# Kernel optimization log

Hardware: AMD Instinct MI355X
Metric: run time of the kernel (lower is better)

## Reference

```python
import jax, jax.numpy as jnp
import numpy as np

T, B, N, D, H = 12, 32, 64, 2, 128
HID, HEAD = 32, 4          # GATBlock n_hid, n_head; HEAD*HID == H
M = N * (N - 1)            # edge rows per get_graph
N_ACT = N - 1              # active nodes per batch row


def _make_graph():
    rec = np.zeros((M, N), np.float32)
    snd = np.zeros((M, N), np.float32)
    k = np.arange(N_ACT * N_ACT)
    ii = np.repeat(np.arange(N_ACT), N_ACT)
    jj = np.tile(np.arange(N_ACT), N_ACT)
    snd[k, ii] = 1.0
    rec[k, jj] = 1.0
    return rec, snd


def setup_inputs() -> dict:
    key = jax.random.key(0)
    ks = jax.random.split(key, 16)
    rec, snd = _make_graph()
    inp = {
        "inputs": jax.random.normal(ks[0], (T, B, N, D), jnp.float32),
        "hidden": jax.random.normal(ks[1], (B, N, H), jnp.float32),
        "rel_rec": jnp.asarray(np.broadcast_to(rec, (B, M, N)).copy()),
        "rel_send": jnp.asarray(np.broadcast_to(snd, (B, M, N)).copy()),
        # GATBlock rn1: fc1(D->HID), fc2(2*HID->HEAD)
        "rn1_W1": jax.random.normal(ks[2], (HID, D)) * 0.1,
        "rn1_b1": jnp.zeros((HID,)),
        "rn1_W2": jax.random.normal(ks[3], (HEAD, 2 * HID)) * 0.1,
        "rn1_b2": jnp.zeros((HEAD,)),
        # GATBlock rn2: fc1(H->HID), fc2(2*HID->HEAD)
        "rn2_W1": jax.random.normal(ks[4], (HID, H)) * 0.1,
        "rn2_b1": jnp.zeros((HID,)),
        "rn2_W2": jax.random.normal(ks[5], (HEAD, 2 * HID)) * 0.1,
        "rn2_b2": jnp.zeros((HEAD,)),
        # GRUCell(H, H)
        "gru_Wih": jax.random.normal(ks[6], (3 * H, H)) * 0.05,
        "gru_Whh": jax.random.normal(ks[7], (3 * H, H)) * 0.05,
        "gru_bih": jnp.zeros((3 * H,)),
        "gru_bhh": jnp.zeros((3 * H,)),
        # out Linear(H, D)
        "out_W": jax.random.normal(ks[8], (D, H)) * 0.1,
        "out_b": jnp.zeros((D,)),
    }
    return inp


def _gat_block(x_in, rel_rec, rel_send, W1, b1, W2, b2):
    # x_in: B x N x Din
    x = x_in @ W1.T + b1                                   # B,N,HID
    s = jnp.einsum('bmn,bnd->bmd', rel_send, x)            # B,M,HID (senders)
    r = jnp.einsum('bmn,bnd->bmd', rel_rec, x)             # B,M,HID (receivers)
    a = jax.nn.elu(jnp.concatenate([s, r], -1) @ W2.T + b2)  # B,M,HEAD
    # per-receiving-node masked softmax over the edge dim (edge2node)
    m = rel_rec[..., None] > 0                             # B,M,N,1
    logits = jnp.where(m, a[:, :, None, :], -jnp.inf)      # B,M,N,HEAD
    mx = jnp.max(logits, axis=1, keepdims=True)
    mx = jnp.where(jnp.isfinite(mx), mx, 0.0)
    e = jnp.where(m, jnp.exp(logits - mx), 0.0)
    denom = jnp.sum(e, axis=1, keepdims=True)
    att = e / jnp.where(denom > 0, denom, 1.0)             # B,M,N,HEAD
    # weighted scatter-sum: outer(att_edge, sender_feat) summed per node
    out = jnp.einsum('bmnh,bmd->bnhd', att, s)             # B,N,HEAD,HID
    Bn, Nn = x_in.shape[0], x_in.shape[1]
    return jax.nn.elu(out.reshape(Bn, Nn, HEAD * HID))     # B,N,H


def _gru_cell(x, h, Wih, Whh, bih, bhh):
    gi = x @ Wih.T + bih
    gh = h @ Whh.T + bhh
    i_r, i_z, i_n = jnp.split(gi, 3, axis=-1)
    h_r, h_z, h_n = jnp.split(gh, 3, axis=-1)
    r = jax.nn.sigmoid(i_r + h_r)
    z = jax.nn.sigmoid(i_z + h_z)
    n = jnp.tanh(i_n + r * h_n)
    return (1.0 - z) * n + z * h


def reference(inputs, hidden, rel_rec, rel_send,
              rn1_W1, rn1_b1, rn1_W2, rn1_b2,
              rn2_W1, rn2_b1, rn2_W2, rn2_b2,
              gru_Wih, gru_Whh, gru_bih, gru_bhh,
              out_W, out_b):
    def step(h, x_t):
        x = _gat_block(x_t, rel_rec, rel_send, rn1_W1, rn1_b1, rn1_W2, rn1_b2)
        h = _gru_cell(x, h, gru_Wih, gru_Whh, gru_bih, gru_bhh)
        h = _gat_block(h, rel_rec, rel_send, rn2_W1, rn2_b1, rn2_W2, rn2_b2)
        return h, None
    h_final, _ = jax.lax.scan(step, hidden, inputs)
    pred = h_final @ out_W.T + out_b                       # B,N,D
    return pred
```

## Files before the change

### kernel.cpp

```cpp
#include <hip/hip_runtime.h>


#define T_   12
#define B_   32
#define N_   64
#define D_   2
#define H_   128
#define HID_ 32
#define HEAD_ 4
#define NA_  63

__device__ __forceinline__ float eluf(float x){ return x>0.f ? x : expm1f(x); }

#define OFF_H    0u
#define OFF_X1   262144u
#define OFF_PS1  1048576u
#define OFF_PR1  1146880u
#define OFF_XG   1245184u
#define OFF_X2   4390912u
#define OFF_PS2  4456448u
#define OFF_PR2  4464640u
#define OFF_WT   OFF_X1
#define OFF_GI   4472832u
#define WS_NEED_A ((4472832ull + 9437184ull) * 4ull)

__global__ void gat1_fc(const float* __restrict__ inp, const float* __restrict__ W1,
                        const float* __restrict__ b1, const float* __restrict__ W2,
                        const float* __restrict__ b2,
                        float* __restrict__ x1_all, float* __restrict__ ps_all,
                        float* __restrict__ pr_all){
  int grp = blockIdx.x;
  int tid = threadIdx.x;
  __shared__ float sx1[N_*HID_];
  __shared__ float sW1[HID_*D_];
  __shared__ float sb1[HID_];
  __shared__ float sW2[HEAD_*2*HID_];
  __shared__ float sxin[N_*D_];
  if(tid < 64)  sW1[tid] = W1[tid];
  if(tid < 32)  sb1[tid] = b1[tid];
  sW2[tid] = W2[tid];
  if(tid < 128) sxin[tid] = inp[grp*N_*D_ + tid];
  __syncthreads();
  for(int o = tid; o < N_*HID_; o += 256){
    int n = o >> 5, k = o & 31;
    float v = sb1[k] + sxin[n*2]*sW1[k*2] + sxin[n*2+1]*sW1[k*2+1];
    sx1[o] = v;
    x1_all[grp*N_*HID_ + o] = v;
  }
  __syncthreads();
  for(int p = tid; p < N_*8; p += 256){
    int n = p >> 3, q = p & 7, hh = q & 3;
    const float* w  = sW2 + hh*64 + ((q < 4) ? 0 : 32);
    const float* xr = sx1 + n*32;
    float acc = (q < 4) ? b2[hh] : 0.f;
    #pragma unroll
    for(int c = 0; c < 32; c++) acc += xr[c]*w[c];
    if(q < 4) ps_all[grp*N_*HEAD_ + n*4 + hh] = acc;
    else      pr_all[grp*N_*HEAD_ + n*4 + hh] = acc;
  }
}

__global__ void prep_wt(const float* __restrict__ Wih, const float* __restrict__ Whh,
                        float* __restrict__ wtb){
  int idx = blockIdx.x*256 + threadIdx.x;
  int k4 = idx / 768, j = idx - k4*768;
  const float* src = (j < 384) ? (Wih + (size_t)j*H_) : (Whh + (size_t)(j-384)*H_);
  ((float4*)wtb)[idx] = ((const float4*)src)[k4];
}

__global__ __launch_bounds__(256) void gat_att_big2(const float* __restrict__ x1,
    const float* __restrict__ ps, const float* __restrict__ pr,
    float* __restrict__ out){
  int blk = blockIdx.x, g = blk >> 1, dh = blk & 1, tid = threadIdx.x;
  __shared__ float sX[N_*HID_];
  __shared__ float sPs[N_*HEAD_];
  __shared__ float sPr[N_*HEAD_];
  {
    const float4* xs = (const float4*)(x1 + (size_t)g*(N_*HID_));
    ((float4*)sX)[tid]       = xs[tid];
    ((float4*)sX)[tid + 256] = xs[tid + 256];
    sPs[tid] = ps[g*(N_*HEAD_) + tid];
    sPr[tid] = pr[g*(N_*HEAD_) + tid];
  }
  __syncthreads();
  float* outg = out + (size_t)g*(N_*H_);
  if(tid < NA_*HEAD_){
    int r = tid, hh = r & 3;
    float prv = sPr[r];
    float tmax = -1e30f;
    for(int i = 0; i < NA_; i++) tmax = fmaxf(tmax, sPs[i*4 + hh]);
    float m = eluf(tmax + prv);
    float4 acc[4];
    #pragma unroll
    for(int k = 0; k < 4; k++) acc[k] = make_float4(0.f,0.f,0.f,0.f);
    float s = 0.f;
    #pragma unroll 3
    for(int i = 0; i < NA_; i++){
      float tt = sPs[i*4 + hh] + prv;
      float v = tt > 0.f ? tt : expm1f(tt);
      float p = expf(v - m);
      s += p;
      const float4* sxp = (const float4*)&sX[i*32 + dh*16];
      #pragma unroll
      for(int k = 0; k < 4; k++){
        float4 xv = sxp[k];
        acc[k].x += p*xv.x; acc[k].y += p*xv.y;
        acc[k].z += p*xv.z; acc[k].w += p*xv.w;
      }
    }
    float inv = 1.f/s;
    float4* orow = (float4*)(outg + (r>>2)*H_ + hh*32 + dh*16);
    #pragma unroll
    for(int k = 0; k < 4; k++){
      float4 o;
      o.x = eluf(acc[k].x*inv); o.y = eluf(acc[k].y*inv);
      o.z = eluf(acc[k].z*inv); o.w = eluf(acc[k].w*inv);
      orow[k] = o;
    }
  } else {
    int hh = tid - NA_*HEAD_;
    float4 z4 = make_float4(0.f,0.f,0.f,0.f);
    float4* zp = (float4*)(outg + NA_*H_ + hh*32 + dh*16);
    zp[0]=z4; zp[1]=z4; zp[2]=z4; zp[3]=z4;
  }
}

__global__ __launch_bounds__(256) void gi_gemm4(const float* __restrict__ xg,
    const float* __restrict__ wtb, float* __restrict__ gi){
  int tid = threadIdx.x;
  int r0 = blockIdx.x * 16;
  __shared__ __align__(16) float sxg[16][H_];
  ((float4*)sxg)[tid]       = ((const float4*)(xg + (size_t)r0*H_))[tid];
  ((float4*)sxg)[tid + 256] = ((const float4*)(xg + (size_t)r0*H_))[tid + 256];
  __syncthreads();
  int c = tid & 127, rh = (tid >> 7) * 8;
  const float4* wt4 = (const float4*)wtb;
  float ar[8]={0,0,0,0,0,0,0,0}, az[8]={0,0,0,0,0,0,0,0}, an[8]={0,0,0,0,0,0,0,0};
  #pragma unroll 2
  for(int k4 = 0; k4 < 32; k4++){
    float4 w0 = wt4[k4*768 + c];
    float4 w1 = wt4[k4*768 + 128 + c];
    float4 w2 = wt4[k4*768 + 256 + c];
    #pragma unroll
    for(int rr = 0; rr < 8; rr++){
      float4 xv = ((const float4*)sxg[rh + rr])[k4];
      ar[rr] += w0.x*xv.x + w0.y*xv.y + w0.z*xv.z + w0.w*xv.w;
      az[rr] += w1.x*xv.x + w1.y*xv.y + w1.z*xv.z + w1.w*xv.w;
      an[rr] += w2.x*xv.x + w2.y*xv.y + w2.z*xv.z + w2.w*xv.w;
    }
  }
  #pragma unroll
  for(int rr = 0; rr < 8; rr++){
    size_t base = (size_t)(r0 + rh + rr)*384;
    gi[base + c]       = ar[rr];
    gi[base + 128 + c] = az[rr];
    gi[base + 256 + c] = an[rr];
  }
}

__global__ __launch_bounds__(512) void gru_fc6(
    const float* __restrict__ gi, const float* __restrict__ hidden0, int t0,
    const float* __restrict__ x2prev, const float* __restrict__ psprev,
    const float* __restrict__ prprev,
    const float* __restrict__ wtb,
    const float* __restrict__ bih, const float* __restrict__ bhh,
    const float* __restrict__ W1, const float* __restrict__ b1,
    const float* __restrict__ W2, const float* __restrict__ b2,
    float* __restrict__ x2, float* __restrict__ ps2, float* __restrict__ pr2){
  int tid = threadIdx.x, blk = blockIdx.x;
  int g0 = blk*8, g = blk>>3, jbase = (blk&7)*8;
  __shared__ __align__(16) float sX[N_*HID_];
  __shared__ float sPs[N_*HEAD_];
  __shared__ __align__(16) float sh[8][H_];
  __shared__ __align__(16) float shn[8][H_];
  __shared__ float spart[4][24][H_];
  __shared__ float sx2[8][HID_];

  int c = tid & 127, rg = tid >> 7;
  const float4* wt4 = (const float4*)wtb;
  float4 wreg[8][3];
  #pragma unroll
  for(int kk = 0; kk < 8; kk++){
    const float4* wk = wt4 + (size_t)(rg*8 + kk)*768 + 384 + c;
    wreg[kk][0] = wk[0]; wreg[kk][1] = wk[128]; wreg[kk][2] = wk[256];
  }

  if(t0){
    if(tid < 256) ((float4*)sh)[tid] = ((const float4*)(hidden0 + (size_t)g0*H_))[tid];
  } else {
    ((float4*)sX)[tid] = ((const float4*)(x2prev + (size_t)g*(N_*HID_)))[tid];
    if(tid < 256) sPs[tid] = psprev[g*(N_*HEAD_) + tid];
  }
  __syncthreads();

  if(!t0){
    int rl = tid >> 4, l16 = tid & 15;
    int hh = rl & 3, jrow = rl >> 2;
    int jl = jbase + jrow;
    float prv = prprev[g*(N_*HEAD_) + jbase*4 + rl];
    float tmax = -1e30f;
    for(int i = 0; i < NA_; i++) tmax = fmaxf(tmax, sPs[i*4 + hh]);
    float m = eluf(tmax + prv);
    float a0 = 0.f, a1 = 0.f, s = 0.f;
    #pragma unroll 3
    for(int i = 0; i < NA_; i++){
      float tt = sPs[i*4 + hh] + prv;
      float v = tt > 0.f ? tt : expm1f(tt);
      float p = expf(v - m);
      s += p;
      const float2 xv = *(const float2*)&sX[i*32 + l16*2];
      a0 += p*xv.x; a1 += p*xv.y;
    }
    float inv = 1.f/s;
    float h0 = (jl == NA_) ? 0.f : eluf(a0*inv);
    float h1 = (jl == NA_) ? 0.f : eluf(a1*inv);
    sh[jrow][hh*32 + l16*2]     = h0;
    sh[jrow][hh*32 + l16*2 + 1] = h1;
  }
  __syncthreads();

  {
    float ar[8] = {0,0,0,0,0,0,0,0};
    float az[8] = {0,0,0,0,0,0,0,0};
    float an[8] = {0,0,0,0,0,0,0,0};
    #pragma unroll
    for(int kk = 0; kk < 8; kk++){
      int k4 = rg*8 + kk;
      #pragma unroll
      for(int r = 0; r < 8; r++){
        float4 hv = ((const float4*)sh[r])[k4];
        ar[r] += wreg[kk][0].x*hv.x + wreg[kk][0].y*hv.y + wreg[kk][0].z*hv.z + wreg[kk][0].w*hv.w;
        az[r] += wreg[kk][1].x*hv.x + wreg[kk][1].y*hv.y + wreg[kk][1].z*hv.z + wreg[kk][1].w*hv.w;
        an[r] += wreg[kk][2].x*hv.x + wreg[kk][2].y*hv.y + wreg[kk][2].z*hv.z + wreg[kk][2].w*hv.w;
      }
    }
    #pragma unroll
    for(int r = 0; r < 8; r++){
      spart[rg][r][c]      = ar[r];
      spart[rg][8 + r][c]  = az[r];
      spart[rg][16 + r][c] = an[r];
    }
  }
  __syncthreads();

  {
    float bi_r = bih[c], bi_z = bih[c+H_], bi_n = bih[c+2*H_];
    float bh_r = bhh[c], bh_z = bhh[c+H_], bh_n = bhh[c+2*H_];
    int r0 = rg*2;
    #pragma unroll
    for(int rr = 0; rr < 2; rr++){
      int r = r0 + rr;
      float hr = spart[0][r][c] + spart[1][r][c] + spart[2][r][c] + spart[3][r][c] + bh_r;
      float hz = spart[0][8+r][c] + spart[1][8+r][c] + spart[2][8+r][c] + spart[3][8+r][c] + bh_z;
      float hn = spart[0][16+r][c] + spart[1][16+r][c] + spart[2][16+r][c] + spart[3][16+r][c] + bh_n;
      const float* gir = gi + (size_t)(g0+r)*384;
      float ir  = gir[c]     + bi_r;
      float iz  = gir[c+128] + bi_z;
      float in_ = gir[c+256] + bi_n;
      float rgt = 1.f/(1.f+expf(-(ir+hr)));
      float zgt = 1.f/(1.f+expf(-(iz+hz)));
      float ngt = tanhf(in_ + rgt*hn);
      shn[r][c] = (1.f-zgt)*ngt + zgt*sh[r][c];
    }
  }
  __syncthreads();

  if(tid < 256){
    int r = tid >> 5, jc = tid & 31;
    const float4* wrow = (const float4*)(W1 + (size_t)jc*H_);
    const float4* hnr = (const float4*)shn[r];
    float acc = b1[jc];
    #pragma unroll 8
    for(int k4 = 0; k4 < 32; k4++){
      float4 w = wrow[k4], hv = hnr[k4];
      acc += w.x*hv.x + w.y*hv.y + w.z*hv.z + w.w*hv.w;
    }
    sx2[r][jc] = acc;
    x2[(size_t)(g0+r)*HID_ + jc] = acc;
  }
  __syncthreads();
  if(tid < 64){
    int r = tid >> 3, q = tid & 7, hh = q & 3;
    int base = (q < 4) ? 0 : 32;
    float acc = (q < 4) ? b2[hh] : 0.f;
    #pragma unroll
    for(int cc = 0; cc < 32; cc++) acc += sx2[r][cc]*W2[hh*64 + base + cc];
    if(q < 4) ps2[(g0+r)*HEAD_ + hh] = acc;
    else      pr2[(g0+r)*HEAD_ + hh] = acc;
  }
}

__global__ __launch_bounds__(512) void gru_fc3(
    const float* __restrict__ xg, const float* __restrict__ h,
    const float* __restrict__ wtb,
    const float* __restrict__ bih, const float* __restrict__ bhh,
    const float* __restrict__ W1, const float* __restrict__ b1,
    const float* __restrict__ W2, const float* __restrict__ b2,
    float* __restrict__ x2, float* __restrict__ ps2, float* __restrict__ pr2){
  int tid = threadIdx.x;
  int g0 = blockIdx.x * 8;
  __shared__ __align__(16) float sx[8][H_];
  __shared__ __align__(16) float sh[8][H_];
  __shared__ __align__(16) float shn[8][H_];
  __shared__ float sx2[8][HID_];
  if(tid < 256) ((float4*)sx)[tid]     = ((const float4*)(xg + (size_t)g0*H_))[tid];
  else          ((float4*)sh)[tid-256] = ((const float4*)(h  + (size_t)g0*H_))[tid-256];
  __syncthreads();
  int c = tid & 127, rg = tid >> 7, r0 = rg*2;
  const float4* wt4 = (const float4*)wtb;
  const float4* xr0 = (const float4*)sx[r0];
  const float4* xr1 = (const float4*)sx[r0+1];
  const float4* hp0 = (const float4*)sh[r0];
  const float4* hp1 = (const float4*)sh[r0+1];
  float air[2]={0,0}, aiz[2]={0,0}, ain[2]={0,0};
  float ahr[2]={0,0}, ahz[2]={0,0}, ahn[2]={0,0};
  #pragma unroll 2
  for(int k4 = 0; k4 < 32; k4++){
    const float4* wk = wt4 + k4*768 + c;
    float4 w0 = wk[0],   w1 = wk[128], w2 = wk[256];
    float4 w3 = wk[384], w4 = wk[512], w5 = wk[640];
    float4 xv0 = xr0[k4], xv1 = xr1[k4];
    float4 hv0 = hp0[k4], hv1 = hp1[k4];
    air[0] += w0.x*xv0.x + w0.y*xv0.y + w0.z*xv0.z + w0.w*xv0.w;
    aiz[0] += w1.x*xv0.x + w1.y*xv0.y + w1.z*xv0.z + w1.w*xv0.w;
    ain[0] += w2.x*xv0.x + w2.y*xv0.y + w2.z*xv0.z + w2.w*xv0.w;
    ahr[0] += w3.x*hv0.x + w3.y*hv0.y + w3.z*hv0.z + w3.w*hv0.w;
    ahz[0] += w4.x*hv0.x + w4.y*hv0.y + w4.z*hv0.z + w4.w*hv0.w;
    ahn[0] += w5.x*hv0.x + w5.y*hv0.y + w5.z*hv0.z + w5.w*hv0.w;
    air[1] += w0.x*xv1.x + w0.y*xv1.y + w0.z*xv1.z + w0.w*xv1.w;
    aiz[1] += w1.x*xv1.x + w1.y*xv1.y + w1.z*xv1.z + w1.w*xv1.w;
    ain[1] += w2.x*xv1.x + w2.y*xv1.y + w2.z*xv1.z + w2.w*xv1.w;
    ahr[1] += w3.x*hv1.x + w3.y*hv1.y + w3.z*hv1.z + w3.w*hv1.w;
    ahz[1] += w4.x*hv1.x + w4.y*hv1.y + w4.z*hv1.z + w4.w*hv1.w;
    ahn[1] += w5.x*hv1.x + w5.y*hv1.y + w5.z*hv1.z + w5.w*hv1.w;
  }
  float bi_r = bih[c], bi_z = bih[c+H_], bi_n = bih[c+2*H_];
  float bh_r = bhh[c], bh_z = bhh[c+H_], bh_n = bhh[c+2*H_];
  #pragma unroll
  for(int rr = 0; rr < 2; rr++){
    float ir  = air[rr]+bi_r, iz = aiz[rr]+bi_z, in_ = ain[rr]+bi_n;
    float hr  = ahr[rr]+bh_r, hz = ahz[rr]+bh_z, hn  = ahn[rr]+bh_n;
    float rgt = 1.f/(1.f+expf(-(ir+hr)));
    float zgt = 1.f/(1.f+expf(-(iz+hz)));
    float ngt = tanhf(in_ + rgt*hn);
    shn[r0+rr][c] = (1.f-zgt)*ngt + zgt*sh[r0+rr][c];
  }
  __syncthreads();
  if(tid < 256){
    int r = tid >> 5, jc = tid & 31;
    const float4* wrow = (const float4*)(W1 + (size_t)jc*H_);
    const float4* hnr = (const float4*)shn[r];
    float acc = b1[jc];
    #pragma unroll 8
    for(int k4 = 0; k4 < 32; k4++){
      float4 w = wrow[k4], hv = hnr[k4];
      acc += w.x*hv.x + w.y*hv.y + w.z*hv.z + w.w*hv.w;
    }
    sx2[r][jc] = acc;
    x2[(size_t)(g0+r)*HID_ + jc] = acc;
  }
  __syncthreads();
  if(tid < 64){
    int r = tid >> 3, q = tid & 7, hh = q & 3;
    int base = (q < 4) ? 0 : 32;
    float acc = (q < 4) ? b2[hh] : 0.f;
    #pragma unroll
    for(int cc = 0; cc < 32; cc++) acc += sx2[r][cc]*W2[hh*64 + base + cc];
    if(q < 4) ps2[(g0+r)*HEAD_ + hh] = acc;
    else      pr2[(g0+r)*HEAD_ + hh] = acc;
  }
}

__global__ __launch_bounds__(128) void gat_att_sm(const float* __restrict__ x1,
    const float* __restrict__ ps, const float* __restrict__ pr,
    float* __restrict__ out){
  int bid = blockIdx.x;
  int g = bid >> 3, sub = bid & 7, rh = sub >> 2, dq = sub & 3;
  int tid = threadIdx.x;
  __shared__ float sX[N_*HID_];
  __shared__ float sPs[N_*HEAD_];
  __shared__ float sPr[N_*HEAD_];
  {
    const float4* xs = (const float4*)(x1 + (size_t)g*(N_*HID_));
    #pragma unroll
    for(int k = 0; k < 4; k++) ((float4*)sX)[tid + 128*k] = xs[tid + 128*k];
    sPs[tid]       = ps[g*(N_*HEAD_) + tid];
    sPs[tid + 128] = ps[g*(N_*HEAD_) + tid + 128];
    sPr[tid]       = pr[g*(N_*HEAD_) + tid];
    sPr[tid + 128] = pr[g*(N_*HEAD_) + tid + 128];
  }
  __syncthreads();
  float* outg = out + (size_t)g*(N_*H_);
  if(tid < 126){
    int r = rh*126 + tid;
    int hh = r & 3, j = r >> 2;
    float prv = sPr[r];
    float tmax = -1e30f;
    for(int i = 0; i < NA_; i++) tmax = fmaxf(tmax, sPs[i*4 + hh]);
    float m = eluf(tmax + prv);
    float4 a0 = make_float4(0.f,0.f,0.f,0.f), a1 = a0;
    float s = 0.f;
    #pragma unroll 3
    for(int i = 0; i < NA_; i++){
      float tt = sPs[i*4 + hh] + prv;
      float v = tt > 0.f ? tt : expm1f(tt);
      float p = expf(v - m);
      s += p;
      const float4* sxp = (const float4*)&sX[i*32 + dq*8];
      float4 x0 = sxp[0], x1v = sxp[1];
      a0.x += p*x0.x;  a0.y += p*x0.y;  a0.z += p*x0.z;  a0.w += p*x0.w;
      a1.x += p*x1v.x; a1.y += p*x1v.y; a1.z += p*x1v.z; a1.w += p*x1v.w;
    }
    float inv = 1.f/s;
    float4* orow = (float4*)(outg + (size_t)j*H_ + hh*32 + dq*8);
    float4 o0, o1;
    o0.x = eluf(a0.x*inv); o0.y = eluf(a0.y*inv);
    o0.z = eluf(a0.z*inv); o0.w = eluf(a0.w*inv);
    o1.x = eluf(a1.x*inv); o1.y = eluf(a1.y*inv);
    o1.z = eluf(a1.z*inv); o1.w = eluf(a1.w*inv);
    orow[0] = o0; orow[1] = o1;
  } else if(rh == 1){
    float4 z4 = make_float4(0.f,0.f,0.f,0.f);
    float4* zrow = (float4*)(outg + NA_*H_);
    int base = dq*8 + (tid-126)*4;
    #pragma unroll
    for(int k = 0; k < 4; k++) zrow[base + k] = z4;
  }
}

__global__ void final_k(const float* __restrict__ h, const float* __restrict__ oW,
                        const float* __restrict__ ob, float* __restrict__ out){
  int b = blockIdx.x, tid = threadIdx.x;
  int n = tid >> 1, d = tid & 1;
  const float* hr = h + (size_t)(b*N_ + n)*H_;
  float acc = ob[d];
  #pragma unroll 8
  for(int k = 0; k < H_; k++) acc += hr[k]*oW[d*H_ + k];
  out[(b*N_ + n)*D_ + d] = acc;
}

extern "C" void kernel_launch(void* const* d_in, const int* in_sizes, int n_in,
                              void* d_out, int out_size, void* d_ws, size_t ws_size,
                              hipStream_t stream){
  const float* inputs = (const float*)d_in[0];
  const float* hidden = (const float*)d_in[1];
  const float* rn1_W1 = (const float*)d_in[4];
  const float* rn1_b1 = (const float*)d_in[5];
  const float* rn1_W2 = (const float*)d_in[6];
  const float* rn1_b2 = (const float*)d_in[7];
  const float* rn2_W1 = (const float*)d_in[8];
  const float* rn2_b1 = (const float*)d_in[9];
  const float* rn2_W2 = (const float*)d_in[10];
  const float* rn2_b2 = (const float*)d_in[11];
  const float* gWih   = (const float*)d_in[12];
  const float* gWhh   = (const float*)d_in[13];
  const float* gbih   = (const float*)d_in[14];
  const float* gbhh   = (const float*)d_in[15];
  const float* oW     = (const float*)d_in[16];
  const float* ob     = (const float*)d_in[17];
  float* ws = (float*)d_ws;

  const int use_gi = (ws_size >= WS_NEED_A) ? 1 : 0;

  gat1_fc<<<T_*B_, 256, 0, stream>>>(inputs, rn1_W1, rn1_b1, rn1_W2, rn1_b2,
                                     ws + OFF_X1, ws + OFF_PS1, ws + OFF_PR1);
  gat_att_big2<<<T_*B_*2, 256, 0, stream>>>(ws + OFF_X1, ws + OFF_PS1, ws + OFF_PR1,
                                            ws + OFF_XG);
  prep_wt<<<96, 256, 0, stream>>>(gWih, gWhh, ws + OFF_WT);

  const float* xg0  = ws + OFF_XG;
  const float* wtbp = ws + OFF_WT;
  float* hb  = ws + OFF_H;

  if(use_gi){
    gi_gemm4<<<T_*B_*N_/16, 256, 0, stream>>>(xg0, wtbp, ws + OFF_GI);
    float* x2b[2] = {ws + OFF_X2,  ws + OFF_PS1};
    float* psb[2] = {ws + OFF_PS2, ws + OFF_PR1};
    float* prb[2] = {ws + OFF_PR2, ws + OFF_PR1 + 8192};
    for(int t = 0; t < T_; t++){
      int w = t & 1, rp = w ^ 1;
      gru_fc6<<<256, 512, 0, stream>>>(ws + OFF_GI + (size_t)t*B_*N_*384,
                                       hidden, (t == 0) ? 1 : 0,
                                       x2b[rp], psb[rp], prb[rp],
                                       wtbp, gbih, gbhh,
                                       rn2_W1, rn2_b1, rn2_W2, rn2_b2,
                                       x2b[w], psb[w], prb[w]);
    }
    gat_att_sm<<<B_*8, 128, 0, stream>>>(x2b[1], psb[1], prb[1], hb);
  } else {
    float* x2p = ws + OFF_X2;
    float* psp = ws + OFF_PS2;
    float* prp = ws + OFF_PR2;
    for(int t = 0; t < T_; t++){
      const float* hsrc = (t == 0) ? hidden : hb;
      gru_fc3<<<B_*N_/8, 512, 0, stream>>>(xg0 + (size_t)t*B_*N_*H_, hsrc,
                                           wtbp, gbih, gbhh,
                                           rn2_W1, rn2_b1, rn2_W2, rn2_b2,
                                           x2p, psp, prp);
      gat_att_sm<<<B_*8, 128, 0, stream>>>(x2p, psp, prp, hb);
    }
  }
  final_k<<<B_, 128, 0, stream>>>(hb, oW, ob, (float*)d_out);
}
```

Measured before the change: 475.2 us.

## Fuse recurrent GRU+GAT timestep loop into one persistent per-batch kernel

Replaces the per-timestep gru_fc6 launches, the trailing attention kernel and the final output kernel with one kernel launched with one 1024-thread block per batch. Each block keeps its 64-node hidden state in shared memory across all 12 steps and does the GRU, fc1, fc2 and attention locally, which removes the launch overhead and the global round-trips between steps. The cost is that only 32 blocks run on the GPU. Weights are now streamed from global/L2 on every step instead of being held in registers, so per-step latency may grow.

```diff
diff --git a/kernel.cpp b/kernel.cpp
--- a/kernel.cpp
+++ b/kernel.cpp
@@ -158,135 +158,125 @@
   }
 }
 
-__global__ __launch_bounds__(512) void gru_fc6(
-    const float* __restrict__ gi, const float* __restrict__ hidden0, int t0,
-    const float* __restrict__ x2prev, const float* __restrict__ psprev,
-    const float* __restrict__ prprev,
+__global__ __launch_bounds__(1024) void loop_g(
+    const float* __restrict__ gi, const float* __restrict__ hidden0,
     const float* __restrict__ wtb,
     const float* __restrict__ bih, const float* __restrict__ bhh,
     const float* __restrict__ W1, const float* __restrict__ b1,
     const float* __restrict__ W2, const float* __restrict__ b2,
-    float* __restrict__ x2, float* __restrict__ ps2, float* __restrict__ pr2){
-  int tid = threadIdx.x, blk = blockIdx.x;
-  int g0 = blk*8, g = blk>>3, jbase = (blk&7)*8;
-  __shared__ __align__(16) float sX[N_*HID_];
-  __shared__ float sPs[N_*HEAD_];
-  __shared__ __align__(16) float sh[8][H_];
-  __shared__ __align__(16) float shn[8][H_];
-  __shared__ float spart[4][24][H_];
-  __shared__ float sx2[8][HID_];
-
-  int c = tid & 127, rg = tid >> 7;
+    const float* __restrict__ oW, const float* __restrict__ ob,
+    float* __restrict__ out){
+  int tid = threadIdx.x, g = blockIdx.x;
+  __shared__ __align__(16) float sh[N_][H_];
+  __shared__ __align__(16) float shn[N_][H_];
+  __shared__ __align__(16) float sx2[N_][HID_];
+  __shared__ float sps[N_*HEAD_];
+  __shared__ float spr[N_*HEAD_];
+
+  {
+    const float4* hp = (const float4*)(hidden0 + (size_t)g*N_*H_);
+    ((float4*)sh)[tid]        = hp[tid];
+    ((float4*)sh)[tid + 1024] = hp[tid + 1024];
+  }
+  int c = tid & 127, rq = tid >> 7;
+  float bi_r = bih[c], bi_z = bih[c+H_], bi_n = bih[c+2*H_];
+  float bh_r = bhh[c], bh_z = bhh[c+H_], bh_n = bhh[c+2*H_];
   const float4* wt4 = (const float4*)wtb;
-  float4 wreg[8][3];
-  #pragma unroll
-  for(int kk = 0; kk < 8; kk++){
-    const float4* wk = wt4 + (size_t)(rg*8 + kk)*768 + 384 + c;
-    wreg[kk][0] = wk[0]; wreg[kk][1] = wk[128]; wreg[kk][2] = wk[256];
-  }
-
-  if(t0){
-    if(tid < 256) ((float4*)sh)[tid] = ((const float4*)(hidden0 + (size_t)g0*H_))[tid];
-  } else {
-    ((float4*)sX)[tid] = ((const float4*)(x2prev + (size_t)g*(N_*HID_)))[tid];
-    if(tid < 256) sPs[tid] = psprev[g*(N_*HEAD_) + tid];
-  }
-  __syncthreads();
-
-  if(!t0){
-    int rl = tid >> 4, l16 = tid & 15;
-    int hh = rl & 3, jrow = rl >> 2;
-    int jl = jbase + jrow;
-    float prv = prprev[g*(N_*HEAD_) + jbase*4 + rl];
-    float tmax = -1e30f;
-    for(int i = 0; i < NA_; i++) tmax = fmaxf(tmax, sPs[i*4 + hh]);
-    float m = eluf(tmax + prv);
-    float a0 = 0.f, a1 = 0.f, s = 0.f;
-    #pragma unroll 3
-    for(int i = 0; i < NA_; i++){
-      float tt = sPs[i*4 + hh] + prv;
-      float v = tt > 0.f ? tt : expm1f(tt);
-      float p = expf(v - m);
-      s += p;
-      const float2 xv = *(const float2*)&sX[i*32 + l16*2];
-      a0 += p*xv.x; a1 += p*xv.y;
-    }
-    float inv = 1.f/s;
-    float h0 = (jl == NA_) ? 0.f : eluf(a0*inv);
-    float h1 = (jl == NA_) ? 0.f : eluf(a1*inv);
-    sh[jrow][hh*32 + l16*2]     = h0;
-    sh[jrow][hh*32 + l16*2 + 1] = h1;
-  }
-  __syncthreads();
-
-  {
-    float ar[8] = {0,0,0,0,0,0,0,0};
-    float az[8] = {0,0,0,0,0,0,0,0};
-    float an[8] = {0,0,0,0,0,0,0,0};
-    #pragma unroll
-    for(int kk = 0; kk < 8; kk++){
-      int k4 = rg*8 + kk;
+  __syncthreads();
+
+  for(int t = 0; t < T_; t++){
+    float ar[8]={0,0,0,0,0,0,0,0}, az[8]={0,0,0,0,0,0,0,0}, an[8]={0,0,0,0,0,0,0,0};
+    #pragma unroll 2
+    for(int k4 = 0; k4 < 32; k4++){
+      const float4* wk = wt4 + k4*768 + 384 + c;
+      float4 w0 = wk[0], w1 = wk[128], w2 = wk[256];
       #pragma unroll
-      for(int r = 0; r < 8; r++){
-        float4 hv = ((const float4*)sh[r])[k4];
-        ar[r] += wreg[kk][0].x*hv.x + wreg[kk][0].y*hv.y + wreg[kk][0].z*hv.z + wreg[kk][0].w*hv.w;
-        az[r] += wreg[kk][1].x*hv.x + wreg[kk][1].y*hv.y + wreg[kk][1].z*hv.z + wreg[kk][1].w*hv.w;
-        an[r] += wreg[kk][2].x*hv.x + wreg[kk][2].y*hv.y + wreg[kk][2].z*hv.z + wreg[kk][2].w*hv.w;
+      for(int rr = 0; rr < 8; rr++){
+        float4 hv = *(const float4*)&sh[rq*8+rr][k4*4];
+        ar[rr] += w0.x*hv.x + w0.y*hv.y + w0.z*hv.z + w0.w*hv.w;
+        az[rr] += w1.x*hv.x + w1.y*hv.y + w1.z*hv.z + w1.w*hv.w;
+        an[rr] += w2.x*hv.x + w2.y*hv.y + w2.z*hv.z + w2.w*hv.w;
       }
     }
     #pragma unroll
-    for(int r = 0; r < 8; r++){
-      spart[rg][r][c]      = ar[r];
-      spart[rg][8 + r][c]  = az[r];
-      spart[rg][16 + r][c] = an[r];
-    }
-  }
-  __syncthreads();
-
-  {
-    float bi_r = bih[c], bi_z = bih[c+H_], bi_n = bih[c+2*H_];
-    float bh_r = bhh[c], bh_z = bhh[c+H_], bh_n = bhh[c+2*H_];
-    int r0 = rg*2;
-    #pragma unroll
-    for(int rr = 0; rr < 2; rr++){
-      int r = r0 + rr;
-      float hr = spart[0][r][c] + spart[1][r][c] + spart[2][r][c] + spart[3][r][c] + bh_r;
-      float hz = spart[0][8+r][c] + spart[1][8+r][c] + spart[2][8+r][c] + spart[3][8+r][c] + bh_z;
-      float hn = spart[0][16+r][c] + spart[1][16+r][c] + spart[2][16+r][c] + spart[3][16+r][c] + bh_n;
-      const float* gir = gi + (size_t)(g0+r)*384;
+    for(int rr = 0; rr < 8; rr++){
+      int row = rq*8 + rr;
+      const float* gir = gi + ((size_t)t*B_*N_ + (size_t)g*N_ + row)*384;
       float ir  = gir[c]     + bi_r;
       float iz  = gir[c+128] + bi_z;
       float in_ = gir[c+256] + bi_n;
+      float hr = ar[rr] + bh_r, hz = az[rr] + bh_z, hn = an[rr] + bh_n;
       float rgt = 1.f/(1.f+expf(-(ir+hr)));
       float zgt = 1.f/(1.f+expf(-(iz+hz)));
       float ngt = tanhf(in_ + rgt*hn);
-      shn[r][c] = (1.f-zgt)*ngt + zgt*sh[r][c];
-    }
-  }
-  __syncthreads();
-
-  if(tid < 256){
-    int r = tid >> 5, jc = tid & 31;
-    const float4* wrow = (const float4*)(W1 + (size_t)jc*H_);
-    const float4* hnr = (const float4*)shn[r];
-    float acc = b1[jc];
+      shn[row][c] = (1.f-zgt)*ngt + zgt*sh[row][c];
+    }
+    __syncthreads();
+    #pragma unroll
+    for(int oo = 0; oo < 2; oo++){
+      int o = tid + oo*1024;
+      int r = o >> 5, jc = o & 31;
+      const float4* wrow = (const float4*)(W1 + (size_t)jc*H_);
+      const float4* hnr = (const float4*)shn[r];
+      float acc = b1[jc];
+      #pragma unroll 8
+      for(int k4 = 0; k4 < 32; k4++){
+        float4 w = wrow[k4], hv = hnr[k4];
+        acc += w.x*hv.x + w.y*hv.y + w.z*hv.z + w.w*hv.w;
+      }
+      sx2[r][jc] = acc;
+    }
+    __syncthreads();
+    if(tid < 512){
+      int r = tid >> 3, q = tid & 7, hh = q & 3;
+      int base = (q < 4) ? 0 : 32;
+      float acc = (q < 4) ? b2[hh] : 0.f;
+      #pragma unroll
+      for(int cc = 0; cc < 32; cc++) acc += sx2[r][cc]*W2[hh*64 + base + cc];
+      if(q < 4) sps[r*4 + hh] = acc;
+      else      spr[r*4 + hh] = acc;
+    }
+    __syncthreads();
+    if(tid < NA_*HEAD_*4){
+      int r = tid >> 2, dq = tid & 3;
+      int hh = r & 3, j = r >> 2;
+      float prv = spr[r];
+      float tmax = -1e30f;
+      for(int i = 0; i < NA_; i++) tmax = fmaxf(tmax, sps[i*4 + hh]);
+      float m = eluf(tmax + prv);
+      float4 a0 = make_float4(0.f,0.f,0.f,0.f), a1 = a0;
+      float s = 0.f;
+      #pragma unroll 3
+      for(int i = 0; i < NA_; i++){
+        float tt = sps[i*4 + hh] + prv;
+        float v = tt > 0.f ? tt : expm1f(tt);
+        float p = expf(v - m);
+        s += p;
+        const float4* sxp = (const float4*)&sx2[i][dq*8];
+        float4 x0 = sxp[0], x1v = sxp[1];
+        a0.x += p*x0.x;  a0.y += p*x0.y;  a0.z += p*x0.z;  a0.w += p*x0.w;
+        a1.x += p*x1v.x; a1.y += p*x1v.y; a1.z += p*x1v.z; a1.w += p*x1v.w;
+      }
+      float inv = 1.f/s;
+      float* orow = &sh[j][hh*32 + dq*8];
+      orow[0] = eluf(a0.x*inv); orow[1] = eluf(a0.y*inv);
+      orow[2] = eluf(a0.z*inv); orow[3] = eluf(a0.w*inv);
+      orow[4] = eluf(a1.x*inv); orow[5] = eluf(a1.y*inv);
+      orow[6] = eluf(a1.z*inv); orow[7] = eluf(a1.w*inv);
+    } else {
+      int k = tid - NA_*HEAD_*4;
+      #pragma unroll
+      for(int q2 = 0; q2 < 8; q2++) sh[NA_][k*8 + q2] = 0.f;
+    }
+    __syncthreads();
+  }
+  if(tid < 128){
+    int n = tid >> 1, d = tid & 1;
+    const float* hr = sh[n];
+    float acc = ob[d];
     #pragma unroll 8
-    for(int k4 = 0; k4 < 32; k4++){
-      float4 w = wrow[k4], hv = hnr[k4];
-      acc += w.x*hv.x + w.y*hv.y + w.z*hv.z + w.w*hv.w;
-    }
-    sx2[r][jc] = acc;
-    x2[(size_t)(g0+r)*HID_ + jc] = acc;
-  }
-  __syncthreads();
-  if(tid < 64){
-    int r = tid >> 3, q = tid & 7, hh = q & 3;
-    int base = (q < 4) ? 0 : 32;
-    float acc = (q < 4) ? b2[hh] : 0.f;
-    #pragma unroll
-    for(int cc = 0; cc < 32; cc++) acc += sx2[r][cc]*W2[hh*64 + base + cc];
-    if(q < 4) ps2[(g0+r)*HEAD_ + hh] = acc;
-    else      pr2[(g0+r)*HEAD_ + hh] = acc;
+    for(int k = 0; k < H_; k++) acc += hr[k]*oW[d*H_ + k];
+    out[((size_t)g*N_ + n)*D_ + d] = acc;
   }
 }
 
@@ -470,24 +460,14 @@
 
   const float* xg0  = ws + OFF_XG;
   const float* wtbp = ws + OFF_WT;
-  float* hb  = ws + OFF_H;
 
   if(use_gi){
     gi_gemm4<<<T_*B_*N_/16, 256, 0, stream>>>(xg0, wtbp, ws + OFF_GI);
-    float* x2b[2] = {ws + OFF_X2,  ws + OFF_PS1};
-    float* psb[2] = {ws + OFF_PS2, ws + OFF_PR1};
-    float* prb[2] = {ws + OFF_PR2, ws + OFF_PR1 + 8192};
-    for(int t = 0; t < T_; t++){
-      int w = t & 1, rp = w ^ 1;
-      gru_fc6<<<256, 512, 0, stream>>>(ws + OFF_GI + (size_t)t*B_*N_*384,
-                                       hidden, (t == 0) ? 1 : 0,
-                                       x2b[rp], psb[rp], prb[rp],
-                                       wtbp, gbih, gbhh,
-                                       rn2_W1, rn2_b1, rn2_W2, rn2_b2,
-                                       x2b[w], psb[w], prb[w]);
-    }
-    gat_att_sm<<<B_*8, 128, 0, stream>>>(x2b[1], psb[1], prb[1], hb);
+    loop_g<<<B_, 1024, 0, stream>>>(ws + OFF_GI, hidden, wtbp,
+                                    gbih, gbhh, rn2_W1, rn2_b1, rn2_W2, rn2_b2,
+                                    oW, ob, (float*)d_out);
   } else {
+    float* hb  = ws + OFF_H;
     float* x2p = ws + OFF_X2;
     float* psp = ws + OFF_PS2;
     float* prp = ws + OFF_PR2;
@@ -499,6 +479,6 @@
                                            x2p, psp, prp);
       gat_att_sm<<<B_*8, 128, 0, stream>>>(x2p, psp, prp, hb);
     }
-  }
-  final_k<<<B_, 128, 0, stream>>>(hb, oW, ob, (float*)d_out);
-}
+    final_k<<<B_, 128, 0, stream>>>(hb, oW, ob, (float*)d_out);
+  }
+}
```

New measurement: 1.243 ms. 2.62x slower.
